# Optimization experiments

Measured on AMD Instinct MI355X. Metric: run time of the kernel, lower is better.

Reference implementation:

```python
import jax, jax.numpy as jnp
import numpy as np

N = 50000      # nodes
E = 800000     # directed edges (before self-loops)
F_IN = 128     # input features
HID = 64       # hidden channels per head (conv1)
HEADS = 4      # attention heads (conv1)
C = 47         # num classes (conv2 out, 1 output head, concat=False)
NEG_SLOPE = 0.2


def _glorot(key, shape):
    fan = shape[0] + shape[-1] if len(shape) > 1 else shape[-1]
    lim = float(np.sqrt(6.0 / fan))
    return jax.random.uniform(key, shape, jnp.float32, -lim, lim)


def setup_inputs() -> dict:
    key = jax.random.key(0)
    ks = jax.random.split(key, 10)
    x = jax.random.normal(ks[0], (N, F_IN), jnp.float32)
    edge_index = jax.random.randint(ks[1], (2, E), 0, N, jnp.int32)
    W1 = _glorot(ks[2], (F_IN, HEADS * HID))
    a_src1 = _glorot(ks[3], (HEADS, HID))
    a_dst1 = _glorot(ks[4], (HEADS, HID))
    b1 = jnp.zeros((HEADS * HID,), jnp.float32)
    W2 = _glorot(ks[5], (HEADS * HID, 1 * C))
    a_src2 = _glorot(ks[6], (1, C))
    a_dst2 = _glorot(ks[7], (1, C))
    b2 = jnp.zeros((C,), jnp.float32)
    return {"x": x, "edge_index": edge_index, "W1": W1, "a_src1": a_src1,
            "a_dst1": a_dst1, "b1": b1, "W2": W2, "a_src2": a_src2,
            "a_dst2": a_dst2, "b2": b2}


def _gat_conv(x, W, a_src, a_dst, b, src, dst, n, heads, out_ch, concat):
    # linear transform, split heads: [n, heads, out_ch]
    h = (x @ W).reshape(n, heads, out_ch)
    # per-node attention logits
    al_s = jnp.sum(h * a_src, axis=-1)            # [n, heads]
    al_d = jnp.sum(h * a_dst, axis=-1)            # [n, heads]
    # per-edge scores (messages flow src -> dst)
    e = jax.nn.leaky_relu(al_s[src] + al_d[dst], NEG_SLOPE)  # [E', heads]
    # scatter-softmax over edges sharing a destination node
    e_max = jax.ops.segment_max(e, dst, num_segments=n)      # [n, heads]
    ex = jnp.exp(e - e_max[dst])
    denom = jax.ops.segment_sum(ex, dst, num_segments=n)
    alpha = ex / (denom[dst] + 1e-16)                        # [E', heads]
    # attention-weighted scatter-add aggregation
    out = jax.ops.segment_sum(h[src] * alpha[:, :, None], dst, num_segments=n)
    out = out.reshape(n, heads * out_ch) if concat else jnp.mean(out, axis=1)
    return out + b


def reference(x, edge_index, W1, a_src1, a_dst1, b1, W2, a_src2, a_dst2, b2):
    n = x.shape[0]
    # add self-loops (PyG GATConv default)
    loops = jnp.arange(n, dtype=edge_index.dtype)
    src = jnp.concatenate([edge_index[0], loops])
    dst = jnp.concatenate([edge_index[1], loops])
    # dropout omitted (eval mode)
    h = jax.nn.elu(_gat_conv(x, W1, a_src1, a_dst1, b1, src, dst, n, HEADS, HID, True))
    out = _gat_conv(h, W2, a_src2, a_dst2, b2, src, dst, n, 1, C, False)
    return jax.nn.log_softmax(out, axis=1)
```

## Files before the change

### kernel.cpp

```cpp
#include <hip/hip_runtime.h>
#include <hip/hip_fp16.h>
#include <math.h>

#define N_NODES 50000
#define E_EDGES 800000
#define E_TOT   850000
#define F_IN    128
#define C1      256
#define NCLS    47
#define H2S     48
#define NEG     0.2f
#define SCAN_B  196

typedef _Float16 f16x8 __attribute__((ext_vector_type(8)));
typedef float    f32x4 __attribute__((ext_vector_type(4)));


__global__ void k_count(const int* __restrict__ ei, int* __restrict__ deg) {
    int i = blockIdx.x * 256 + threadIdx.x;
    if (i >= E_TOT) return;
    int dst = (i < E_EDGES) ? ei[E_EDGES + i] : (i - E_EDGES);
    atomicAdd(&deg[dst], 1);
}

__global__ void k_scan_blk(const int* __restrict__ deg, int* __restrict__ blksum) {
    __shared__ int ws[4];
    int i = blockIdx.x * 256 + threadIdx.x;
    int v = (i < N_NODES) ? deg[i] : 0;
    int lane = threadIdx.x & 63, w = threadIdx.x >> 6;
    #pragma unroll
    for (int off = 32; off; off >>= 1) v += __shfl_xor(v, off);
    if (lane == 0) ws[w] = v;
    __syncthreads();
    if (threadIdx.x == 0) blksum[blockIdx.x] = ws[0] + ws[1] + ws[2] + ws[3];
}

__global__ void k_scan_top(const int* __restrict__ blksum, int* __restrict__ blkoff) {
    __shared__ int ws[4];
    int tid = threadIdx.x, lane = tid & 63, w = tid >> 6;
    int v = (tid < SCAN_B) ? blksum[tid] : 0;
    int sc = v;
    #pragma unroll
    for (int off = 1; off < 64; off <<= 1) {
        int t = __shfl_up(sc, off);
        if (lane >= off) sc += t;
    }
    if (lane == 63) ws[w] = sc;
    __syncthreads();
    if (tid == 0) { int a = 0; for (int t = 0; t < 4; t++) { int u = ws[t]; ws[t] = a; a += u; } }
    __syncthreads();
    if (tid < SCAN_B) blkoff[tid] = sc + ws[w] - v;
}

__global__ void k_scan_fin(const int* __restrict__ deg, const int* __restrict__ blkoff,
                           int* __restrict__ row_ptr, int* __restrict__ cursor) {
    __shared__ int ws[4];
    int i = blockIdx.x * 256 + threadIdx.x;
    int v = (i < N_NODES) ? deg[i] : 0;
    int lane = threadIdx.x & 63, w = threadIdx.x >> 6;
    int sc = v;
    #pragma unroll
    for (int off = 1; off < 64; off <<= 1) {
        int t = __shfl_up(sc, off);
        if (lane >= off) sc += t;
    }
    if (lane == 63) ws[w] = sc;
    __syncthreads();
    if (threadIdx.x == 0) { int a = 0; for (int t = 0; t < 4; t++) { int u = ws[t]; ws[t] = a; a += u; } }
    __syncthreads();
    int incl = sc + ws[w] + blkoff[blockIdx.x];
    if (i < N_NODES) {
        row_ptr[i + 1] = incl;
        cursor[i]      = incl - v;
    }
    if (i == 0) row_ptr[0] = 0;
}

__global__ void k_scatter(const int* __restrict__ ei, int* __restrict__ cursor,
                          int* __restrict__ csr_src) {
    int i = blockIdx.x * 256 + threadIdx.x;
    if (i >= E_TOT) return;
    int src, dst;
    if (i < E_EDGES) { src = ei[i]; dst = ei[E_EDGES + i]; }
    else             { src = dst = i - E_EDGES; }
    int pos = atomicAdd(&cursor[dst], 1);
    csr_src[pos] = src;
}


__global__ void k_prepx(const float* __restrict__ x, __half* __restrict__ xh) {
    int i = blockIdx.x * 256 + threadIdx.x;
    if (i >= N_NODES * F_IN / 4) return;
    float4 v = ((const float4*)x)[i];
    ushort4 p;
    p.x = __half_as_ushort(__float2half_rn(v.x));
    p.y = __half_as_ushort(__float2half_rn(v.y));
    p.z = __half_as_ushort(__float2half_rn(v.z));
    p.w = __half_as_ushort(__float2half_rn(v.w));
    ((ushort4*)xh)[i] = p;
}


__global__ void k_prepw1f(const float* __restrict__ W1, uint4* __restrict__ W1f) {
    int t = blockIdx.x * 256 + threadIdx.x;
    if (t >= 4096) return;
    int f = t >> 8, ks = (t >> 6) & 3, lane = t & 63;
    int c  = f * 16 + (lane & 15);
    int kb = ks * 32 + ((lane >> 4) << 3);
    unsigned short h[8];
    #pragma unroll
    for (int j = 0; j < 8; j++)
        h[j] = __half_as_ushort(__float2half_rn(W1[(size_t)(kb + j) * C1 + c]));
    W1f[t] = make_uint4((unsigned)h[0] | ((unsigned)h[1] << 16),
                        (unsigned)h[2] | ((unsigned)h[3] << 16),
                        (unsigned)h[4] | ((unsigned)h[5] << 16),
                        (unsigned)h[6] | ((unsigned)h[7] << 16));
}


__global__ void k_prepw2f(const float* __restrict__ W2, uint4* __restrict__ W2f) {
    int t = blockIdx.x * 256 + threadIdx.x;
    if (t >= 1536) return;
    int f = t >> 9, ks = (t >> 6) & 7, lane = t & 63;
    int c  = f * 16 + (lane & 15);
    int kb = ks * 32 + ((lane >> 4) << 3);
    unsigned short h[8];
    #pragma unroll
    for (int j = 0; j < 8; j++) {
        float v = (c < NCLS) ? W2[(size_t)(kb + j) * NCLS + c] : 0.f;
        h[j] = __half_as_ushort(__float2half_rn(v));
    }
    W2f[t] = make_uint4((unsigned)h[0] | ((unsigned)h[1] << 16),
                        (unsigned)h[2] | ((unsigned)h[3] << 16),
                        (unsigned)h[4] | ((unsigned)h[5] << 16),
                        (unsigned)h[6] | ((unsigned)h[7] << 16));
}


__global__ void __launch_bounds__(64)
k_gemm1(const __half* __restrict__ xh, const uint4* __restrict__ W1f,
        const float* __restrict__ a_src1, const float* __restrict__ a_dst1,
        __half* __restrict__ H1h, float* __restrict__ al_s, float* __restrict__ al_d) {
    int lane = threadIdx.x;
    int n0 = blockIdx.x * 16;
    const __half* aptr = xh + (size_t)(n0 + (lane & 15)) * F_IN + ((lane >> 4) << 3);
    const f16x8* bptr = (const f16x8*)W1f;
    f32x4 acc[16];
    #pragma unroll
    for (int f = 0; f < 16; f++) acc[f] = (f32x4){0.f, 0.f, 0.f, 0.f};
    #pragma unroll
    for (int ks = 0; ks < 4; ks++) {
        f16x8 a = *(const f16x8*)(aptr + ks * 32);
        #pragma unroll
        for (int f = 0; f < 16; f++) {
            f16x8 b = bptr[(f * 4 + ks) * 64 + lane];
            acc[f] = __builtin_amdgcn_mfma_f32_16x16x32_f16(a, b, acc[f], 0, 0, 0);
        }
    }
    int col = lane & 15;
    int g4  = (lane >> 4) * 4;
    float asf[16], adf[16];
    #pragma unroll
    for (int f = 0; f < 16; f++) {
        asf[f] = a_src1[f * 16 + col];
        adf[f] = a_dst1[f * 16 + col];
    }
    #pragma unroll
    for (int reg = 0; reg < 4; reg++) {
        int n = n0 + g4 + reg;
        float vs[4] = {0.f, 0.f, 0.f, 0.f};
        float vd[4] = {0.f, 0.f, 0.f, 0.f};
        #pragma unroll
        for (int f = 0; f < 16; f++) {
            float v = acc[f][reg];
            H1h[(size_t)n * C1 + f * 16 + col] = __float2half_rn(v);
            vs[f >> 2] += v * asf[f];
            vd[f >> 2] += v * adf[f];
        }
        #pragma unroll
        for (int h = 0; h < 4; h++) {
            #pragma unroll
            for (int off = 8; off; off >>= 1) {
                vs[h] += __shfl_xor(vs[h], off);
                vd[h] += __shfl_xor(vd[h], off);
            }
        }
        if (col == 0) {
            #pragma unroll
            for (int h = 0; h < 4; h++) {
                al_s[n * 4 + h] = vs[h];
                al_d[n * 4 + h] = vd[h];
            }
        }
    }
}


__global__ void k_agg1(const __half* __restrict__ H1h, const float* __restrict__ al_s,
                       const float* __restrict__ al_d, const int* __restrict__ row_ptr,
                       const int* __restrict__ csr_src, const float* __restrict__ b1,
                       __half* __restrict__ HEh) {
    int n = blockIdx.x * 4 + (threadIdx.x >> 6);
    int lane = threadIdx.x & 63;
    int h = lane >> 4;
    int beg = row_ptr[n], end = row_ptr[n + 1];
    float ald = al_d[n * 4 + h];
    float m = -INFINITY, s = 0.f;
    float a0 = 0.f, a1 = 0.f, a2 = 0.f, a3 = 0.f;
    int j = beg;
    for (; j + 3 < end; j += 4) {
        int ss[4]; float ee[4]; ushort4 hh[4];
        #pragma unroll
        for (int t = 0; t < 4; t++) ss[t] = csr_src[j + t];
        #pragma unroll
        for (int t = 0; t < 4; t++) ee[t] = al_s[ss[t] * 4 + h];
        #pragma unroll
        for (int t = 0; t < 4; t++)
            hh[t] = *(const ushort4*)(H1h + (size_t)ss[t] * C1 + lane * 4);
        #pragma unroll
        for (int t = 0; t < 4; t++) {
            float e = ee[t] + ald;
            ee[t] = (e >= 0.f) ? e : NEG * e;
        }
        float nm = fmaxf(m, fmaxf(fmaxf(ee[0], ee[1]), fmaxf(ee[2], ee[3])));
        float f = __expf(m - nm);
        m = nm;
        float p[4];
        #pragma unroll
        for (int t = 0; t < 4; t++) p[t] = __expf(ee[t] - nm);
        s = s * f + p[0] + p[1] + p[2] + p[3];
        a0 *= f; a1 *= f; a2 *= f; a3 *= f;
        #pragma unroll
        for (int t = 0; t < 4; t++) {
            a0 += p[t] * __half2float(__ushort_as_half(hh[t].x));
            a1 += p[t] * __half2float(__ushort_as_half(hh[t].y));
            a2 += p[t] * __half2float(__ushort_as_half(hh[t].z));
            a3 += p[t] * __half2float(__ushort_as_half(hh[t].w));
        }
    }
    for (; j < end; j++) {
        int s0 = csr_src[j];
        float e = al_s[s0 * 4 + h] + ald;
        e = (e >= 0.f) ? e : NEG * e;
        ushort4 hv = *(const ushort4*)(H1h + (size_t)s0 * C1 + lane * 4);
        float nm = fmaxf(m, e);
        float f  = __expf(m - nm);
        float pr = __expf(e - nm);
        s  = s  * f + pr;
        a0 = a0 * f + pr * __half2float(__ushort_as_half(hv.x));
        a1 = a1 * f + pr * __half2float(__ushort_as_half(hv.y));
        a2 = a2 * f + pr * __half2float(__ushort_as_half(hv.z));
        a3 = a3 * f + pr * __half2float(__ushort_as_half(hv.w));
        m = nm;
    }
    float inv = 1.f / (s + 1e-16f);
    float4 bb = *(const float4*)(b1 + lane * 4);
    float o0 = a0 * inv + bb.x, o1 = a1 * inv + bb.y;
    float o2 = a2 * inv + bb.z, o3 = a3 * inv + bb.w;
    o0 = (o0 > 0.f) ? o0 : expm1f(o0);
    o1 = (o1 > 0.f) ? o1 : expm1f(o1);
    o2 = (o2 > 0.f) ? o2 : expm1f(o2);
    o3 = (o3 > 0.f) ? o3 : expm1f(o3);
    ushort4 pk;
    pk.x = __half_as_ushort(__float2half_rn(o0));
    pk.y = __half_as_ushort(__float2half_rn(o1));
    pk.z = __half_as_ushort(__float2half_rn(o2));
    pk.w = __half_as_ushort(__float2half_rn(o3));
    *(ushort4*)(HEh + (size_t)n * C1 + lane * 4) = pk;
}


__global__ void __launch_bounds__(64)
k_gemm2(const __half* __restrict__ HEh, const uint4* __restrict__ W2f,
        const float* __restrict__ a_src2, const float* __restrict__ a_dst2,
        __half* __restrict__ H2h, float* __restrict__ al_s2, float* __restrict__ al_d2) {
    int lane = threadIdx.x;
    int n0 = blockIdx.x * 16;
    const __half* aptr = HEh + (size_t)(n0 + (lane & 15)) * C1 + ((lane >> 4) << 3);
    const f16x8* bptr = (const f16x8*)W2f;
    f32x4 acc0 = {0.f, 0.f, 0.f, 0.f};
    f32x4 acc1 = {0.f, 0.f, 0.f, 0.f};
    f32x4 acc2 = {0.f, 0.f, 0.f, 0.f};
    #pragma unroll
    for (int ks = 0; ks < 8; ks++) {
        f16x8 a  = *(const f16x8*)(aptr + ks * 32);
        f16x8 b0 = bptr[(0 * 8 + ks) * 64 + lane];
        f16x8 b1 = bptr[(1 * 8 + ks) * 64 + lane];
        f16x8 b2 = bptr[(2 * 8 + ks) * 64 + lane];
        acc0 = __builtin_amdgcn_mfma_f32_16x16x32_f16(a, b0, acc0, 0, 0, 0);
        acc1 = __builtin_amdgcn_mfma_f32_16x16x32_f16(a, b1, acc1, 0, 0, 0);
        acc2 = __builtin_amdgcn_mfma_f32_16x16x32_f16(a, b2, acc2, 0, 0, 0);
    }
    int col = lane & 15;
    int g4  = (lane >> 4) * 4;
    float as[3], ad[3];
    #pragma unroll
    for (int f = 0; f < 3; f++) {
        int c = f * 16 + col;
        as[f] = (c < NCLS) ? a_src2[c] : 0.f;
        ad[f] = (c < NCLS) ? a_dst2[c] : 0.f;
    }
    #pragma unroll
    for (int reg = 0; reg < 4; reg++) {
        int n = n0 + g4 + reg;
        float v0 = acc0[reg], v1 = acc1[reg], v2 = acc2[reg];
        __half* orow = H2h + (size_t)n * H2S;
        orow[col]      = __float2half_rn(v0);
        orow[16 + col] = __float2half_rn(v1);
        orow[32 + col] = __float2half_rn(v2);
        float vs = v0 * as[0] + v1 * as[1] + v2 * as[2];
        float vd = v0 * ad[0] + v1 * ad[1] + v2 * ad[2];
        #pragma unroll
        for (int off = 8; off; off >>= 1) {
            vs += __shfl_xor(vs, off);
            vd += __shfl_xor(vd, off);
        }
        if (col == 0) { al_s2[n] = vs; al_d2[n] = vd; }
    }
}


__global__ void k_agg2(const __half* __restrict__ H2h, const float* __restrict__ al_s2,
                       const float* __restrict__ al_d2, const int* __restrict__ row_ptr,
                       const int* __restrict__ csr_src, const float* __restrict__ b2,
                       float* __restrict__ out) {
    int n = blockIdx.x * 4 + (threadIdx.x >> 6);
    if (n >= N_NODES) return;
    int lane = threadIdx.x & 63;
    int beg = row_ptr[n], end = row_ptr[n + 1];
    float ald = al_d2[n];
    float m = -INFINITY, s = 0.f, acc = 0.f;
    int j = beg;
    for (; j + 3 < end; j += 4) {
        int ss[4]; float ee[4]; float hv[4];
        #pragma unroll
        for (int t = 0; t < 4; t++) ss[t] = csr_src[j + t];
        #pragma unroll
        for (int t = 0; t < 4; t++) ee[t] = al_s2[ss[t]];
        #pragma unroll
        for (int t = 0; t < 4; t++)
            hv[t] = (lane < NCLS) ? __half2float(H2h[(size_t)ss[t] * H2S + lane]) : 0.f;
        #pragma unroll
        for (int t = 0; t < 4; t++) {
            float e = ee[t] + ald;
            ee[t] = (e >= 0.f) ? e : NEG * e;
        }
        float nm = fmaxf(m, fmaxf(fmaxf(ee[0], ee[1]), fmaxf(ee[2], ee[3])));
        float f = __expf(m - nm);
        m = nm;
        float p[4];
        #pragma unroll
        for (int t = 0; t < 4; t++) p[t] = __expf(ee[t] - nm);
        s = s * f + p[0] + p[1] + p[2] + p[3];
        acc = acc * f + p[0] * hv[0] + p[1] * hv[1] + p[2] * hv[2] + p[3] * hv[3];
    }
    for (; j < end; j++) {
        int src = csr_src[j];
        float e = al_s2[src] + ald;
        e = (e >= 0.f) ? e : NEG * e;
        float hv = (lane < NCLS) ? __half2float(H2h[(size_t)src * H2S + lane]) : 0.f;
        float nm = fmaxf(m, e);
        float f  = __expf(m - nm);
        float pr = __expf(e - nm);
        s   = s   * f + pr;
        acc = acc * f + pr * hv;
        m = nm;
    }
    float v = acc / (s + 1e-16f) + ((lane < NCLS) ? b2[lane] : -INFINITY);
    float mx = v;
    #pragma unroll
    for (int off = 32; off; off >>= 1) mx = fmaxf(mx, __shfl_xor(mx, off));
    float ex = __expf(v - mx);
    float sum = ex;
    #pragma unroll
    for (int off = 32; off; off >>= 1) sum += __shfl_xor(sum, off);
    if (lane < NCLS) out[(size_t)n * NCLS + lane] = v - mx - logf(sum);
}


extern "C" void kernel_launch(void* const* d_in, const int* in_sizes, int n_in,
                              void* d_out, int out_size, void* d_ws, size_t ws_size,
                              hipStream_t stream) {
    const float* x      = (const float*)d_in[0];
    const int*   ei     = (const int*)  d_in[1];
    const float* W1     = (const float*)d_in[2];
    const float* a_src1 = (const float*)d_in[3];
    const float* a_dst1 = (const float*)d_in[4];
    const float* b1     = (const float*)d_in[5];
    const float* W2     = (const float*)d_in[6];
    const float* a_src2 = (const float*)d_in[7];
    const float* a_dst2 = (const float*)d_in[8];
    const float* b2     = (const float*)d_in[9];
    float* out = (float*)d_out;

    char* base = (char*)d_ws;
    size_t off = 0;
    auto alloc = [&](size_t bytes) -> void* {
        void* r = base + off;
        off += (bytes + 511) & ~size_t(511);
        return r;
    };
    __half* H1h   = (__half*)alloc((size_t)N_NODES * C1 * 2);
    __half* HEh   = (__half*)alloc((size_t)N_NODES * C1 * 2);
    __half* H2h   = (__half*)alloc((size_t)N_NODES * H2S * 2);
    __half* xh    = (__half*)alloc((size_t)N_NODES * F_IN * 2);
    uint4*  W1f   = (uint4*) alloc((size_t)4096 * 16);
    uint4*  W2f   = (uint4*) alloc((size_t)1536 * 16);
    float*  al_s1 = (float*) alloc((size_t)N_NODES * 4 * 4);
    float*  al_d1 = (float*) alloc((size_t)N_NODES * 4 * 4);
    float*  al_s2 = (float*) alloc((size_t)N_NODES * 4);
    float*  al_d2 = (float*) alloc((size_t)N_NODES * 4);
    int*    deg   = (int*)   alloc((size_t)N_NODES * 4);
    int*    rowp  = (int*)   alloc((size_t)(N_NODES + 1) * 4);
    int*    cursor= (int*)   alloc((size_t)N_NODES * 4);
    int*    blks  = (int*)   alloc((size_t)SCAN_B * 4);
    int*    blko  = (int*)   alloc((size_t)SCAN_B * 4);
    int*    csrs  = (int*)   alloc((size_t)E_TOT * 4);

    hipMemsetAsync(deg, 0, (size_t)N_NODES * 4, stream);

    int eb = (E_TOT + 255) / 256;
    k_count   <<<eb, 256, 0, stream>>>(ei, deg);
    k_scan_blk<<<SCAN_B, 256, 0, stream>>>(deg, blks);
    k_scan_top<<<1, 256, 0, stream>>>(blks, blko);
    k_scan_fin<<<SCAN_B, 256, 0, stream>>>(deg, blko, rowp, cursor);
    k_scatter <<<eb, 256, 0, stream>>>(ei, cursor, csrs);
    k_prepx   <<<(N_NODES * F_IN / 4 + 255) / 256, 256, 0, stream>>>(x, xh);
    k_prepw1f <<<16, 256, 0, stream>>>(W1, W1f);
    k_prepw2f <<<6, 256, 0, stream>>>(W2, W2f);

    k_gemm1<<<N_NODES / 16, 64, 0, stream>>>(xh, W1f, a_src1, a_dst1, H1h, al_s1, al_d1);
    k_agg1 <<<(N_NODES + 3) / 4, 256, 0, stream>>>(H1h, al_s1, al_d1, rowp, csrs, b1, HEh);
    k_gemm2<<<N_NODES / 16, 64, 0, stream>>>(HEh, W2f, a_src2, a_dst2, H2h, al_s2, al_d2);
    k_agg2 <<<(N_NODES + 3) / 4, 256, 0, stream>>>(H2h, al_s2, al_d2, rowp, csrs, b2, out);
}
```

Baseline: 349.1 us.

## Fuse layer-1 aggregation with layer-2 GEMM and merge setup kernels

Layer-1 attention aggregation now writes its ELU outputs for 16 nodes into shared memory, and one wavefront runs the layer-2 MFMA GEMM on them in the same 1024-thread block. This removes the 25.6MB HEh round trip through global memory and one launch. The degree count, x conversion and weight repacking are also merged into a single block-range-dispatched setup kernel. In exchange, 15 of 16 wavefronts sit idle during the GEMM phase, and the large blocks can leave load imbalance when degrees vary.

```diff
diff --git a/kernel.cpp b/kernel.cpp
--- a/kernel.cpp
+++ b/kernel.cpp
@@ -11,17 +11,76 @@
 #define H2S     48
 #define NEG     0.2f
 #define SCAN_B  196
+#define HEP     264
+
+#define SB_CNT  3321
+#define SB_PX   6250
+#define SB_W1   16
+#define SB_W2   6
 
 typedef _Float16 f16x8 __attribute__((ext_vector_type(8)));
 typedef float    f32x4 __attribute__((ext_vector_type(4)));
 
 
-__global__ void k_count(const int* __restrict__ ei, int* __restrict__ deg) {
-    int i = blockIdx.x * 256 + threadIdx.x;
-    if (i >= E_TOT) return;
-    int dst = (i < E_EDGES) ? ei[E_EDGES + i] : (i - E_EDGES);
-    atomicAdd(&deg[dst], 1);
-}
+__global__ void k_setup(const int* __restrict__ ei, int* __restrict__ deg,
+                        const float* __restrict__ x, __half* __restrict__ xh,
+                        const float* __restrict__ W1, uint4* __restrict__ W1f,
+                        const float* __restrict__ W2, uint4* __restrict__ W2f) {
+    int bid = blockIdx.x;
+    if (bid < SB_CNT) {
+        int i = bid * 256 + threadIdx.x;
+        if (i >= E_TOT) return;
+        int dst = (i < E_EDGES) ? ei[E_EDGES + i] : (i - E_EDGES);
+        atomicAdd(&deg[dst], 1);
+        return;
+    }
+    bid -= SB_CNT;
+    if (bid < SB_PX) {
+        int i = bid * 256 + threadIdx.x;
+        float4 v = ((const float4*)x)[i];
+        ushort4 p;
+        p.x = __half_as_ushort(__float2half_rn(v.x));
+        p.y = __half_as_ushort(__float2half_rn(v.y));
+        p.z = __half_as_ushort(__float2half_rn(v.z));
+        p.w = __half_as_ushort(__float2half_rn(v.w));
+        ((ushort4*)xh)[i] = p;
+        return;
+    }
+    bid -= SB_PX;
+    if (bid < SB_W1) {
+        int t = bid * 256 + threadIdx.x;
+        int f = t >> 8, ks = (t >> 6) & 3, lane = t & 63;
+        int c  = f * 16 + (lane & 15);
+        int kb = ks * 32 + ((lane >> 4) << 3);
+        unsigned short h[8];
+        #pragma unroll
+        for (int j = 0; j < 8; j++)
+            h[j] = __half_as_ushort(__float2half_rn(W1[(size_t)(kb + j) * C1 + c]));
+        W1f[t] = make_uint4((unsigned)h[0] | ((unsigned)h[1] << 16),
+                            (unsigned)h[2] | ((unsigned)h[3] << 16),
+                            (unsigned)h[4] | ((unsigned)h[5] << 16),
+                            (unsigned)h[6] | ((unsigned)h[7] << 16));
+        return;
+    }
+    bid -= SB_W1;
+    {
+        int t = bid * 256 + threadIdx.x;
+        int f = t >> 9, ks = (t >> 6) & 7, lane = t & 63;
+        int c  = f * 16 + (lane & 15);
+        int kb = ks * 32 + ((lane >> 4) << 3);
+        unsigned short h[8];
+        #pragma unroll
+        for (int j = 0; j < 8; j++) {
+            float v = (c < NCLS) ? W2[(size_t)(kb + j) * NCLS + c] : 0.f;
+            h[j] = __half_as_ushort(__float2half_rn(v));
+        }
+        W2f[t] = make_uint4((unsigned)h[0] | ((unsigned)h[1] << 16),
+                            (unsigned)h[2] | ((unsigned)h[3] << 16),
+                            (unsigned)h[4] | ((unsigned)h[5] << 16),
+                            (unsigned)h[6] | ((unsigned)h[7] << 16));
+    }
+}
+
 
 __global__ void k_scan_blk(const int* __restrict__ deg, int* __restrict__ blksum) {
     __shared__ int ws[4];
@@ -88,55 +147,6 @@
 }
 
 
-__global__ void k_prepx(const float* __restrict__ x, __half* __restrict__ xh) {
-    int i = blockIdx.x * 256 + threadIdx.x;
-    if (i >= N_NODES * F_IN / 4) return;
-    float4 v = ((const float4*)x)[i];
-    ushort4 p;
-    p.x = __half_as_ushort(__float2half_rn(v.x));
-    p.y = __half_as_ushort(__float2half_rn(v.y));
-    p.z = __half_as_ushort(__float2half_rn(v.z));
-    p.w = __half_as_ushort(__float2half_rn(v.w));
-    ((ushort4*)xh)[i] = p;
-}
-
-
-__global__ void k_prepw1f(const float* __restrict__ W1, uint4* __restrict__ W1f) {
-    int t = blockIdx.x * 256 + threadIdx.x;
-    if (t >= 4096) return;
-    int f = t >> 8, ks = (t >> 6) & 3, lane = t & 63;
-    int c  = f * 16 + (lane & 15);
-    int kb = ks * 32 + ((lane >> 4) << 3);
-    unsigned short h[8];
-    #pragma unroll
-    for (int j = 0; j < 8; j++)
-        h[j] = __half_as_ushort(__float2half_rn(W1[(size_t)(kb + j) * C1 + c]));
-    W1f[t] = make_uint4((unsigned)h[0] | ((unsigned)h[1] << 16),
-                        (unsigned)h[2] | ((unsigned)h[3] << 16),
-                        (unsigned)h[4] | ((unsigned)h[5] << 16),
-                        (unsigned)h[6] | ((unsigned)h[7] << 16));
-}
-
-
-__global__ void k_prepw2f(const float* __restrict__ W2, uint4* __restrict__ W2f) {
-    int t = blockIdx.x * 256 + threadIdx.x;
-    if (t >= 1536) return;
-    int f = t >> 9, ks = (t >> 6) & 7, lane = t & 63;
-    int c  = f * 16 + (lane & 15);
-    int kb = ks * 32 + ((lane >> 4) << 3);
-    unsigned short h[8];
-    #pragma unroll
-    for (int j = 0; j < 8; j++) {
-        float v = (c < NCLS) ? W2[(size_t)(kb + j) * NCLS + c] : 0.f;
-        h[j] = __half_as_ushort(__float2half_rn(v));
-    }
-    W2f[t] = make_uint4((unsigned)h[0] | ((unsigned)h[1] << 16),
-                        (unsigned)h[2] | ((unsigned)h[3] << 16),
-                        (unsigned)h[4] | ((unsigned)h[5] << 16),
-                        (unsigned)h[6] | ((unsigned)h[7] << 16));
-}
-
-
 __global__ void __launch_bounds__(64)
 k_gemm1(const __half* __restrict__ xh, const uint4* __restrict__ W1f,
         const float* __restrict__ a_src1, const float* __restrict__ a_dst1,
@@ -196,126 +206,127 @@
 }
 
 
-__global__ void k_agg1(const __half* __restrict__ H1h, const float* __restrict__ al_s,
-                       const float* __restrict__ al_d, const int* __restrict__ row_ptr,
-                       const int* __restrict__ csr_src, const float* __restrict__ b1,
-                       __half* __restrict__ HEh) {
-    int n = blockIdx.x * 4 + (threadIdx.x >> 6);
+__global__ void __launch_bounds__(1024)
+k_agg1g2(const __half* __restrict__ H1h, const float* __restrict__ al_s,
+         const float* __restrict__ al_d, const int* __restrict__ row_ptr,
+         const int* __restrict__ csr_src, const float* __restrict__ b1,
+         const uint4* __restrict__ W2f, const float* __restrict__ a_src2,
+         const float* __restrict__ a_dst2, __half* __restrict__ H2h,
+         float* __restrict__ al_s2, float* __restrict__ al_d2) {
+    __shared__ __half he[16][HEP];
+    int w = threadIdx.x >> 6;
     int lane = threadIdx.x & 63;
-    int h = lane >> 4;
-    int beg = row_ptr[n], end = row_ptr[n + 1];
-    float ald = al_d[n * 4 + h];
-    float m = -INFINITY, s = 0.f;
-    float a0 = 0.f, a1 = 0.f, a2 = 0.f, a3 = 0.f;
-    int j = beg;
-    for (; j + 3 < end; j += 4) {
-        int ss[4]; float ee[4]; ushort4 hh[4];
-        #pragma unroll
-        for (int t = 0; t < 4; t++) ss[t] = csr_src[j + t];
-        #pragma unroll
-        for (int t = 0; t < 4; t++) ee[t] = al_s[ss[t] * 4 + h];
-        #pragma unroll
-        for (int t = 0; t < 4; t++)
-            hh[t] = *(const ushort4*)(H1h + (size_t)ss[t] * C1 + lane * 4);
-        #pragma unroll
-        for (int t = 0; t < 4; t++) {
-            float e = ee[t] + ald;
-            ee[t] = (e >= 0.f) ? e : NEG * e;
-        }
-        float nm = fmaxf(m, fmaxf(fmaxf(ee[0], ee[1]), fmaxf(ee[2], ee[3])));
-        float f = __expf(m - nm);
-        m = nm;
-        float p[4];
-        #pragma unroll
-        for (int t = 0; t < 4; t++) p[t] = __expf(ee[t] - nm);
-        s = s * f + p[0] + p[1] + p[2] + p[3];
-        a0 *= f; a1 *= f; a2 *= f; a3 *= f;
-        #pragma unroll
-        for (int t = 0; t < 4; t++) {
-            a0 += p[t] * __half2float(__ushort_as_half(hh[t].x));
-            a1 += p[t] * __half2float(__ushort_as_half(hh[t].y));
-            a2 += p[t] * __half2float(__ushort_as_half(hh[t].z));
-            a3 += p[t] * __half2float(__ushort_as_half(hh[t].w));
-        }
-    }
-    for (; j < end; j++) {
-        int s0 = csr_src[j];
-        float e = al_s[s0 * 4 + h] + ald;
-        e = (e >= 0.f) ? e : NEG * e;
-        ushort4 hv = *(const ushort4*)(H1h + (size_t)s0 * C1 + lane * 4);
-        float nm = fmaxf(m, e);
-        float f  = __expf(m - nm);
-        float pr = __expf(e - nm);
-        s  = s  * f + pr;
-        a0 = a0 * f + pr * __half2float(__ushort_as_half(hv.x));
-        a1 = a1 * f + pr * __half2float(__ushort_as_half(hv.y));
-        a2 = a2 * f + pr * __half2float(__ushort_as_half(hv.z));
-        a3 = a3 * f + pr * __half2float(__ushort_as_half(hv.w));
-        m = nm;
-    }
-    float inv = 1.f / (s + 1e-16f);
-    float4 bb = *(const float4*)(b1 + lane * 4);
-    float o0 = a0 * inv + bb.x, o1 = a1 * inv + bb.y;
-    float o2 = a2 * inv + bb.z, o3 = a3 * inv + bb.w;
-    o0 = (o0 > 0.f) ? o0 : expm1f(o0);
-    o1 = (o1 > 0.f) ? o1 : expm1f(o1);
-    o2 = (o2 > 0.f) ? o2 : expm1f(o2);
-    o3 = (o3 > 0.f) ? o3 : expm1f(o3);
-    ushort4 pk;
-    pk.x = __half_as_ushort(__float2half_rn(o0));
-    pk.y = __half_as_ushort(__float2half_rn(o1));
-    pk.z = __half_as_ushort(__float2half_rn(o2));
-    pk.w = __half_as_ushort(__float2half_rn(o3));
-    *(ushort4*)(HEh + (size_t)n * C1 + lane * 4) = pk;
-}
-
-
-__global__ void __launch_bounds__(64)
-k_gemm2(const __half* __restrict__ HEh, const uint4* __restrict__ W2f,
-        const float* __restrict__ a_src2, const float* __restrict__ a_dst2,
-        __half* __restrict__ H2h, float* __restrict__ al_s2, float* __restrict__ al_d2) {
-    int lane = threadIdx.x;
     int n0 = blockIdx.x * 16;
-    const __half* aptr = HEh + (size_t)(n0 + (lane & 15)) * C1 + ((lane >> 4) << 3);
-    const f16x8* bptr = (const f16x8*)W2f;
-    f32x4 acc0 = {0.f, 0.f, 0.f, 0.f};
-    f32x4 acc1 = {0.f, 0.f, 0.f, 0.f};
-    f32x4 acc2 = {0.f, 0.f, 0.f, 0.f};
-    #pragma unroll
-    for (int ks = 0; ks < 8; ks++) {
-        f16x8 a  = *(const f16x8*)(aptr + ks * 32);
-        f16x8 b0 = bptr[(0 * 8 + ks) * 64 + lane];
-        f16x8 b1 = bptr[(1 * 8 + ks) * 64 + lane];
-        f16x8 b2 = bptr[(2 * 8 + ks) * 64 + lane];
-        acc0 = __builtin_amdgcn_mfma_f32_16x16x32_f16(a, b0, acc0, 0, 0, 0);
-        acc1 = __builtin_amdgcn_mfma_f32_16x16x32_f16(a, b1, acc1, 0, 0, 0);
-        acc2 = __builtin_amdgcn_mfma_f32_16x16x32_f16(a, b2, acc2, 0, 0, 0);
-    }
-    int col = lane & 15;
-    int g4  = (lane >> 4) * 4;
-    float as[3], ad[3];
-    #pragma unroll
-    for (int f = 0; f < 3; f++) {
-        int c = f * 16 + col;
-        as[f] = (c < NCLS) ? a_src2[c] : 0.f;
-        ad[f] = (c < NCLS) ? a_dst2[c] : 0.f;
-    }
-    #pragma unroll
-    for (int reg = 0; reg < 4; reg++) {
-        int n = n0 + g4 + reg;
-        float v0 = acc0[reg], v1 = acc1[reg], v2 = acc2[reg];
-        __half* orow = H2h + (size_t)n * H2S;
-        orow[col]      = __float2half_rn(v0);
-        orow[16 + col] = __float2half_rn(v1);
-        orow[32 + col] = __float2half_rn(v2);
-        float vs = v0 * as[0] + v1 * as[1] + v2 * as[2];
-        float vd = v0 * ad[0] + v1 * ad[1] + v2 * ad[2];
-        #pragma unroll
-        for (int off = 8; off; off >>= 1) {
-            vs += __shfl_xor(vs, off);
-            vd += __shfl_xor(vd, off);
-        }
-        if (col == 0) { al_s2[n] = vs; al_d2[n] = vd; }
+    {
+        int n = n0 + w;
+        int h = lane >> 4;
+        int beg = row_ptr[n], end = row_ptr[n + 1];
+        float ald = al_d[n * 4 + h];
+        float m = -INFINITY, s = 0.f;
+        float a0 = 0.f, a1 = 0.f, a2 = 0.f, a3 = 0.f;
+        int j = beg;
+        for (; j + 3 < end; j += 4) {
+            int ss[4]; float ee[4]; ushort4 hh[4];
+            #pragma unroll
+            for (int t = 0; t < 4; t++) ss[t] = csr_src[j + t];
+            #pragma unroll
+            for (int t = 0; t < 4; t++) ee[t] = al_s[ss[t] * 4 + h];
+            #pragma unroll
+            for (int t = 0; t < 4; t++)
+                hh[t] = *(const ushort4*)(H1h + (size_t)ss[t] * C1 + lane * 4);
+            #pragma unroll
+            for (int t = 0; t < 4; t++) {
+                float e = ee[t] + ald;
+                ee[t] = (e >= 0.f) ? e : NEG * e;
+            }
+            float nm = fmaxf(m, fmaxf(fmaxf(ee[0], ee[1]), fmaxf(ee[2], ee[3])));
+            float f = __expf(m - nm);
+            m = nm;
+            float p[4];
+            #pragma unroll
+            for (int t = 0; t < 4; t++) p[t] = __expf(ee[t] - nm);
+            s = s * f + p[0] + p[1] + p[2] + p[3];
+            a0 *= f; a1 *= f; a2 *= f; a3 *= f;
+            #pragma unroll
+            for (int t = 0; t < 4; t++) {
+                a0 += p[t] * __half2float(__ushort_as_half(hh[t].x));
+                a1 += p[t] * __half2float(__ushort_as_half(hh[t].y));
+                a2 += p[t] * __half2float(__ushort_as_half(hh[t].z));
+                a3 += p[t] * __half2float(__ushort_as_half(hh[t].w));
+            }
+        }
+        for (; j < end; j++) {
+            int s0 = csr_src[j];
+            float e = al_s[s0 * 4 + h] + ald;
+            e = (e >= 0.f) ? e : NEG * e;
+            ushort4 hv = *(const ushort4*)(H1h + (size_t)s0 * C1 + lane * 4);
+            float nm = fmaxf(m, e);
+            float f  = __expf(m - nm);
+            float pr = __expf(e - nm);
+            s  = s  * f + pr;
+            a0 = a0 * f + pr * __half2float(__ushort_as_half(hv.x));
+            a1 = a1 * f + pr * __half2float(__ushort_as_half(hv.y));
+            a2 = a2 * f + pr * __half2float(__ushort_as_half(hv.z));
+            a3 = a3 * f + pr * __half2float(__ushort_as_half(hv.w));
+            m = nm;
+        }
+        float inv = 1.f / (s + 1e-16f);
+        float4 bb = *(const float4*)(b1 + lane * 4);
+        float o0 = a0 * inv + bb.x, o1 = a1 * inv + bb.y;
+        float o2 = a2 * inv + bb.z, o3 = a3 * inv + bb.w;
+        o0 = (o0 > 0.f) ? o0 : expm1f(o0);
+        o1 = (o1 > 0.f) ? o1 : expm1f(o1);
+        o2 = (o2 > 0.f) ? o2 : expm1f(o2);
+        o3 = (o3 > 0.f) ? o3 : expm1f(o3);
+        ushort4 pk;
+        pk.x = __half_as_ushort(__float2half_rn(o0));
+        pk.y = __half_as_ushort(__float2half_rn(o1));
+        pk.z = __half_as_ushort(__float2half_rn(o2));
+        pk.w = __half_as_ushort(__float2half_rn(o3));
+        *(ushort4*)&he[w][lane * 4] = pk;
+    }
+    __syncthreads();
+    if (threadIdx.x < 64) {
+        const f16x8* bptr = (const f16x8*)W2f;
+        f32x4 acc0 = {0.f, 0.f, 0.f, 0.f};
+        f32x4 acc1 = {0.f, 0.f, 0.f, 0.f};
+        f32x4 acc2 = {0.f, 0.f, 0.f, 0.f};
+        #pragma unroll
+        for (int ks = 0; ks < 8; ks++) {
+            f16x8 a  = *(const f16x8*)&he[lane & 15][((lane >> 4) << 3) + ks * 32];
+            f16x8 b0 = bptr[(0 * 8 + ks) * 64 + lane];
+            f16x8 b1 = bptr[(1 * 8 + ks) * 64 + lane];
+            f16x8 b2 = bptr[(2 * 8 + ks) * 64 + lane];
+            acc0 = __builtin_amdgcn_mfma_f32_16x16x32_f16(a, b0, acc0, 0, 0, 0);
+            acc1 = __builtin_amdgcn_mfma_f32_16x16x32_f16(a, b1, acc1, 0, 0, 0);
+            acc2 = __builtin_amdgcn_mfma_f32_16x16x32_f16(a, b2, acc2, 0, 0, 0);
+        }
+        int col = lane & 15;
+        int g4  = (lane >> 4) * 4;
+        float as[3], ad[3];
+        #pragma unroll
+        for (int f = 0; f < 3; f++) {
+            int c = f * 16 + col;
+            as[f] = (c < NCLS) ? a_src2[c] : 0.f;
+            ad[f] = (c < NCLS) ? a_dst2[c] : 0.f;
+        }
+        #pragma unroll
+        for (int reg = 0; reg < 4; reg++) {
+            int n = n0 + g4 + reg;
+            float v0 = acc0[reg], v1 = acc1[reg], v2 = acc2[reg];
+            __half* orow = H2h + (size_t)n * H2S;
+            orow[col]      = __float2half_rn(v0);
+            orow[16 + col] = __float2half_rn(v1);
+            orow[32 + col] = __float2half_rn(v2);
+            float vs = v0 * as[0] + v1 * as[1] + v2 * as[2];
+            float vd = v0 * ad[0] + v1 * ad[1] + v2 * ad[2];
+            #pragma unroll
+            for (int off = 8; off; off >>= 1) {
+                vs += __shfl_xor(vs, off);
+                vd += __shfl_xor(vd, off);
+            }
+            if (col == 0) { al_s2[n] = vs; al_d2[n] = vd; }
+        }
     }
 }
 
@@ -401,7 +412,6 @@
         return r;
     };
     __half* H1h   = (__half*)alloc((size_t)N_NODES * C1 * 2);
-    __half* HEh   = (__half*)alloc((size_t)N_NODES * C1 * 2);
     __half* H2h   = (__half*)alloc((size_t)N_NODES * H2S * 2);
     __half* xh    = (__half*)alloc((size_t)N_NODES * F_IN * 2);
     uint4*  W1f   = (uint4*) alloc((size_t)4096 * 16);
@@ -419,18 +429,15 @@
 
     hipMemsetAsync(deg, 0, (size_t)N_NODES * 4, stream);
 
-    int eb = (E_TOT + 255) / 256;
-    k_count   <<<eb, 256, 0, stream>>>(ei, deg);
+    k_setup   <<<SB_CNT + SB_PX + SB_W1 + SB_W2, 256, 0, stream>>>(
+                  ei, deg, x, xh, W1, W1f, W2, W2f);
     k_scan_blk<<<SCAN_B, 256, 0, stream>>>(deg, blks);
     k_scan_top<<<1, 256, 0, stream>>>(blks, blko);
     k_scan_fin<<<SCAN_B, 256, 0, stream>>>(deg, blko, rowp, cursor);
-    k_scatter <<<eb, 256, 0, stream>>>(ei, cursor, csrs);
-    k_prepx   <<<(N_NODES * F_IN / 4 + 255) / 256, 256, 0, stream>>>(x, xh);
-    k_prepw1f <<<16, 256, 0, stream>>>(W1, W1f);
-    k_prepw2f <<<6, 256, 0, stream>>>(W2, W2f);
-
-    k_gemm1<<<N_NODES / 16, 64, 0, stream>>>(xh, W1f, a_src1, a_dst1, H1h, al_s1, al_d1);
-    k_agg1 <<<(N_NODES + 3) / 4, 256, 0, stream>>>(H1h, al_s1, al_d1, rowp, csrs, b1, HEh);
-    k_gemm2<<<N_NODES / 16, 64, 0, stream>>>(HEh, W2f, a_src2, a_dst2, H2h, al_s2, al_d2);
-    k_agg2 <<<(N_NODES + 3) / 4, 256, 0, stream>>>(H2h, al_s2, al_d2, rowp, csrs, b2, out);
-}
+    k_scatter <<<(E_TOT + 255) / 256, 256, 0, stream>>>(ei, cursor, csrs);
+
+    k_gemm1  <<<N_NODES / 16, 64, 0, stream>>>(xh, W1f, a_src1, a_dst1, H1h, al_s1, al_d1);
+    k_agg1g2 <<<N_NODES / 16, 1024, 0, stream>>>(H1h, al_s1, al_d1, rowp, csrs, b1,
+                                                 W2f, a_src2, a_dst2, H2h, al_s2, al_d2);
+    k_agg2   <<<(N_NODES + 3) / 4, 256, 0, stream>>>(H2h, al_s2, al_d2, rowp, csrs, b2, out);
+}
```

Measured after the change: 387.8 us. 1.11x slower.
